# Kernel tuning notes

Hardware: AMD Instinct MI355X
Metric: run time of the kernel (lower is better)

The kernel has to match this reference:

```python
import jax, jax.numpy as jnp
import numpy as np

SAMPLE_NUMS = 9
VIEW_RANGE = 2      # args.max_turn_view_range
TEMP = 0.07         # args.temperature
AVG_EPS = 1e-6      # BertAVG eps
COS_EPS = 1e-8      # torch.cosine_similarity eps


def setup_inputs() -> dict:
    key = jax.random.key(0)
    k0, k1, k2 = jax.random.split(key, 3)
    G, S, H = 8, 512, 768            # groups, max_seq_length, hidden_size
    B = G * SAMPLE_NUMS              # 72 flattened dialogues
    self_output = jax.random.normal(k0, (B, S, H), dtype=jnp.float32)
    attention_mask = jnp.ones((B, S), dtype=jnp.float32)
    qa_ids = jax.random.randint(k1, (B, S), 0, 4, dtype=jnp.int32)
    turn_ids = jnp.sort(jax.random.randint(k2, (B, S), 0, 16, dtype=jnp.int32), axis=-1)
    labels = jnp.zeros((G, SAMPLE_NUMS), dtype=jnp.float32).at[:, 0].set(1.0)
    return {"self_output": self_output, "attention_mask": attention_mask,
            "labels": labels, "qa_ids": qa_ids, "turn_ids": turn_ids}


def _masked_avg(x, m):
    # BertAVG: sum over seq of x*m / (sum(m) + eps)   x:[B,S,H] m:[B,S]
    return jnp.sum(x * m[..., None], axis=1) / (jnp.sum(m, axis=1, keepdims=True) + AVG_EPS)


def _cos(x, y):
    # torch.cosine_similarity over last dim, eps-clamped norms
    dot = jnp.sum(x * y, axis=-1)
    nx = jnp.maximum(jnp.linalg.norm(x, axis=-1), COS_EPS)
    ny = jnp.maximum(jnp.linalg.norm(y, axis=-1), COS_EPS)
    c = dot / (nx * ny)
    c = jnp.where(c == 1.0, jnp.nan, c)   # cos[cos==1] = nan
    return c / TEMP


def _calc_loss(pred, labels):
    return -jnp.nanmean(jax.nn.log_softmax(pred, axis=-1) * labels)


def reference(self_output, attention_mask, labels, qa_ids, turn_ids):
    H = self_output.shape[-1]
    # role masks from qa_ids
    q_mask = ((qa_ids == 1) | (qa_ids == 2)).astype(self_output.dtype)
    a_mask = ((qa_ids == 0) | (qa_ids == 2)).astype(self_output.dtype)
    n_mask = (qa_ids == 3).astype(self_output.dtype)
    q_am = attention_mask * q_mask
    a_am = attention_mask * a_mask
    n_am = attention_mask * n_mask
    q_so = self_output * q_am[..., None]   # [B,S,H]
    a_so = self_output * a_am[..., None]
    n_so = self_output * n_am[..., None]
    # role-masked cross scores [B,S,S]
    q_w = jnp.einsum('bsh,bth->bst', q_so, a_so + n_so)
    a_w = jnp.einsum('bsh,bth->bst', a_so, q_so + n_so)
    n_w = jnp.einsum('bsh,bth->bst', n_so, q_so + a_so)
    # turn-range band mask: |turn_s - turn_t| <= range
    dt = turn_ids[:, :, None] - turn_ids[:, None, :]
    band = (jnp.abs(dt) <= VIEW_RANGE).astype(self_output.dtype)  # [B,S,S]
    filtered_w = (q_w + a_w + n_w) * band
    # cross outputs
    q_co = jnp.einsum('bst,bth->bsh', filtered_w, q_so)
    a_co = jnp.einsum('bst,bth->bsh', filtered_w, a_so)
    n_co = jnp.einsum('bst,bth->bsh', filtered_w, n_so)
    # masked averages
    q_self = _masked_avg(q_so, q_am)
    q_cross = _masked_avg(q_co, a_am + n_am)
    a_self = _masked_avg(a_so, a_am)
    a_cross = _masked_avg(a_co, q_am + n_am)
    n_self = _masked_avg(n_so, n_am)
    n_cross = _masked_avg(n_co, q_am + a_am)
    # [G, sample_nums, H]
    q_self = q_self.reshape(-1, SAMPLE_NUMS, H)
    q_cross = q_cross.reshape(-1, SAMPLE_NUMS, H)
    a_self = a_self.reshape(-1, SAMPLE_NUMS, H)
    a_cross = a_cross.reshape(-1, SAMPLE_NUMS, H)
    n_self = n_self.reshape(-1, SAMPLE_NUMS, H)
    n_cross = n_cross.reshape(-1, SAMPLE_NUMS, H)
    q_output = q_self[:, 0, :]
    a_output = a_self[:, 0, :]
    n_output = n_self[:, 0, :]
    # vectorized over sample axis (replaces the python loop + stack)
    logit_q = _cos(q_self, q_cross)  # [G, sample_nums]
    logit_a = _cos(a_self, a_cross)
    logit_n = _cos(n_self, n_cross)
    stage_loss = (_calc_loss(logit_a, labels) + _calc_loss(logit_q, labels)
                  + _calc_loss(logit_n, labels)) / 3.0
    return (stage_loss, q_output, a_output, n_output)
```

## Files before the change

kernel.cpp:

```cpp
#include <hip/hip_runtime.h>
#include <math.h>

#define BB 72
#define SS 512
#define HH 768
#define GG 8
#define SN 9
#define VR 2
#define NT 16
#define ASL 64
#define NPART 16


__device__ float g_W[(size_t)BB * NT * 4 * HH];
__device__ float g_snum[BB * 3 * HH];
__device__ float g_xpart[(size_t)BB * NPART * 3 * HH];
__device__ float g_logits[3 * BB];

__device__ __forceinline__ void class_masks(float am, int id, float& qv, float& av, float& nv) {
    qv = (id == 1 || id == 2) ? am : 0.0f;
    av = (id == 0 || id == 2) ? am : 0.0f;
    nv = (id == 3) ? am : 0.0f;
}

__global__ void k_gw(const float* __restrict__ x, const float* __restrict__ am,
                     const int* __restrict__ qa, const int* __restrict__ turn) {
    __shared__ float G[4][NT][4][ASL];
    __shared__ int   tn[SS];
    __shared__ float c2[SS];
    __shared__ int   idv[SS];

    const int b = blockIdx.y, hs = blockIdx.x;
    const int tid = threadIdx.x, w = tid >> 6, lane = tid & 63;
    const int h = hs * ASL + lane;

    for (int i = tid; i < SS; i += 256) {
        tn[i] = turn[b * SS + i];
        float a = am[b * SS + i]; c2[i] = a * a;
        idv[i] = qa[b * SS + i];
    }
    {
        float* Gf = &G[0][0][0][0];
        for (int i = tid; i < 4 * NT * 4 * ASL; i += 256) Gf[i] = 0.0f;
    }
    __syncthreads();

    const int s0 = w * (SS / 4);
    const float* xcol = x + (size_t)b * SS * HH + h;
    float r0 = 0, r1 = 0, r2 = 0, r3 = 0;
    int cur = tn[s0];

    float A[8], Bu[8];
#define LOADC(dst, c) { const float* p_ = xcol + (size_t)(s0 + (c) * 8) * HH;  \
    _Pragma("unroll") for (int j_ = 0; j_ < 8; ++j_) dst[j_] = p_[(size_t)j_ * HH]; }
#define FLUSH() { G[w][cur][0][lane] = r0; G[w][cur][1][lane] = r1;            \
                  G[w][cur][2][lane] = r2; G[w][cur][3][lane] = r3;            \
                  r0 = r1 = r2 = r3 = 0.0f; }
#define CONSUME(src, c) { _Pragma("unroll") for (int j_ = 0; j_ < 8; ++j_) {   \
    const int s_ = s0 + (c) * 8 + j_;                                          \
    const int v_ = tn[s_];                                                     \
    if (v_ != cur) { FLUSH(); cur = v_; }                                      \
    const float val_ = src[j_] * c2[s_];                                       \
    const int id_ = idv[s_];                                                   \
    if      (id_ == 0) r0 += val_;                                             \
    else if (id_ == 1) r1 += val_;                                             \
    else if (id_ == 2) r2 += val_;                                             \
    else               r3 += val_; } }

    LOADC(A, 0);
    for (int c = 0; c < 16; c += 2) {
        LOADC(Bu, c + 1);
        CONSUME(A, c);
        if (c + 2 < 16) LOADC(A, c + 2);
        CONSUME(Bu, c + 1);
    }
    FLUSH();
#undef LOADC
#undef FLUSH
#undef CONSUME
    __syncthreads();

    for (int v = w * 4; v < w * 4 + 4; ++v) {
        const int ulo = (v - VR < 0) ? 0 : v - VR;
        const int uhi = (v + VR > NT - 1) ? NT - 1 : v + VR;
        float a0 = 0, a1 = 0, a2 = 0, a3 = 0;
        for (int u = ulo; u <= uhi; ++u) {
#pragma unroll
            for (int wq = 0; wq < 4; ++wq) {
                a0 += G[wq][u][0][lane]; a1 += G[wq][u][1][lane];
                a2 += G[wq][u][2][lane]; a3 += G[wq][u][3][lane];
            }
        }
        float* Wo = g_W + ((size_t)(b * NT + v) * 4) * HH + h;
        Wo[0 * HH] = a0; Wo[1 * HH] = a1; Wo[2 * HH] = a2; Wo[3 * HH] = a3;
    }
    if (w == 0) {
        float t0 = 0, t1 = 0, t2 = 0, t3 = 0;
        for (int u = 0; u < NT; ++u) {
#pragma unroll
            for (int wq = 0; wq < 4; ++wq) {
                t0 += G[wq][u][0][lane]; t1 += G[wq][u][1][lane];
                t2 += G[wq][u][2][lane]; t3 += G[wq][u][3][lane];
            }
        }
        g_snum[(b * 3 + 0) * HH + h] = t1 + t2;
        g_snum[(b * 3 + 1) * HH + h] = t0 + t2;
        g_snum[(b * 3 + 2) * HH + h] = t3;
    }
}

__global__ void k_ct(const float* __restrict__ x, const float* __restrict__ am,
                     const int* __restrict__ qa, const int* __restrict__ turn) {
    __shared__ float Wl[4][HH];
    __shared__ float red[4][3 * HH];
    __shared__ int   tnb[32];
    __shared__ float amb[32];
    __shared__ int   idb[32];

    const int b = blockIdx.y, ts = blockIdx.x, T0 = ts * 32;
    const int tid = threadIdx.x, w = tid >> 6, lane = tid & 63;
    if (tid < 32) {
        tnb[tid] = turn[b * SS + T0 + tid];
        amb[tid] = am[b * SS + T0 + tid];
        idb[tid] = qa[b * SS + T0 + tid];
    }
    __syncthreads();
    const int vlo = tnb[0], vhi = tnb[31];
    const float* xb = x + (size_t)b * SS * HH;

    __align__(16) float xn[3][12];
#pragma unroll
    for (int c = 0; c < 3; ++c)
#pragma unroll
        for (int k = 0; k < 12; ++k) xn[c][k] = 0.0f;

    for (int v = vlo; v <= vhi; ++v) {
        const float* Wg = g_W + ((size_t)(b * NT + v) * 4) * HH;
        for (int i = tid * 4; i < 4 * HH; i += 1024)
            *(float4*)&Wl[0][i] = *(const float4*)(Wg + i);
        __syncthreads();

        for (int it = 0; it < 8; ++it) {
            const int tl = w * 8 + it;
            if (tnb[tl] != v) continue;
            const int t = T0 + tl;
            const float* xr = xb + (size_t)t * HH;
            float4 xt4[3];
            xt4[0] = *(const float4*)(xr + 0 * 256 + lane * 4);
            xt4[1] = *(const float4*)(xr + 1 * 256 + lane * 4);
            xt4[2] = *(const float4*)(xr + 2 * 256 + lane * 4);

            float d[4];
#pragma unroll
            for (int i = 0; i < 4; ++i) {
                float s = 0;
#pragma unroll
                for (int ch = 0; ch < 3; ++ch) {
                    const float4 wv = *(const float4*)&Wl[i][ch * 256 + lane * 4];
                    const float4 xv = xt4[ch];
                    s += xv.x * wv.x + xv.y * wv.y + xv.z * wv.z + xv.w * wv.w;
                }
                d[i] = s;
            }
#pragma unroll
            for (int off = 32; off; off >>= 1) {
#pragma unroll
                for (int i = 0; i < 4; ++i) d[i] += __shfl_xor(d[i], off);
            }
            float qt, at, nt; class_masks(amb[tl], idb[tl], qt, at, nt);
            const float ant = at + nt, qnt = qt + nt, qat = qt + at;
            const float Sqq = d[1] + d[2], Sqa = d[2], Saa = d[0] + d[2], Snn = d[3];
            const float cwq = qt * (ant * Sqa + qnt * Saa + qat * Snn);
            const float cwa = at * (ant * Sqq + qnt * Sqa + qat * Snn);
            const float cwn = nt * (ant * (Sqq + Sqa) + qnt * (Sqa + Saa));

            __align__(16) float xt[12];
            *(float4*)&xt[0] = xt4[0]; *(float4*)&xt[4] = xt4[1]; *(float4*)&xt[8] = xt4[2];
#pragma unroll
            for (int k = 0; k < 12; ++k) {
                xn[0][k] += cwq * xt[k];
                xn[1][k] += cwa * xt[k];
                xn[2][k] += cwn * xt[k];
            }
        }
        __syncthreads();
    }

#pragma unroll
    for (int c = 0; c < 3; ++c) {
#pragma unroll
        for (int ch = 0; ch < 3; ++ch)
            *(float4*)&red[w][c * HH + ch * 256 + lane * 4] = *(float4*)&xn[c][ch * 4];
    }
    __syncthreads();
    float* xo = g_xpart + (size_t)(b * NPART + ts) * 3 * HH;
    for (int idx = tid; idx < 3 * HH; idx += 256)
        xo[idx] = red[0][idx] + red[1][idx] + red[2][idx] + red[3][idx];
}

__global__ void k_cos(const float* __restrict__ am, const int* __restrict__ qa,
                      float* __restrict__ out) {
    const int c = blockIdx.x, b = blockIdx.y, tid = threadIdx.x;
    const int wave = tid >> 6, lane = tid & 63;
    __shared__ float redd[4][3];
    __shared__ float sD[3];

    float q = 0, a = 0, n = 0;
    for (int s = tid; s < SS; s += 256) {
        float m = am[b * SS + s]; int id = qa[b * SS + s];
        float qv, av, nv; class_masks(m, id, qv, av, nv);
        q += qv; a += av; n += nv;
    }
#pragma unroll
    for (int off = 32; off; off >>= 1) {
        q += __shfl_down(q, off); a += __shfl_down(a, off); n += __shfl_down(n, off);
    }
    if (lane == 0) { redd[wave][0] = q; redd[wave][1] = a; redd[wave][2] = n; }
    __syncthreads();
    if (tid == 0) {
        float Q = 0, A = 0, N = 0;
#pragma unroll
        for (int w = 0; w < 4; ++w) { Q += redd[w][0]; A += redd[w][1]; N += redd[w][2]; }
        sD[0] = Q; sD[1] = A; sD[2] = N;
    }
    __syncthreads();
    const float Dq = sD[0], Da = sD[1], Dn = sD[2];
    const float Dself = (c == 0) ? Dq : ((c == 1) ? Da : Dn);
    const float Dcross = (c == 0) ? (Da + Dn) : ((c == 1) ? (Dq + Dn) : (Dq + Da));
    const float invS = 1.0f / (Dself + 1e-6f), invC = 1.0f / (Dcross + 1e-6f);

    float dot = 0, n1 = 0, n2 = 0;
#pragma unroll
    for (int j = 0; j < 3; ++j) {
        const int h = tid + j * 256;
        float sv = g_snum[(b * 3 + c) * HH + h];
        float cv = 0;
        const float* xp = g_xpart + ((size_t)b * NPART * 3 + c) * HH + h;
#pragma unroll
        for (int p = 0; p < NPART; ++p) cv += xp[(size_t)p * 3 * HH];
        sv *= invS; cv *= invC;
        dot += sv * cv; n1 += sv * sv; n2 += cv * cv;
        if (b % SN == 0)
            out[1 + ((size_t)c * GG + b / SN) * HH + h] = sv;
    }
#pragma unroll
    for (int off = 32; off; off >>= 1) {
        dot += __shfl_down(dot, off); n1 += __shfl_down(n1, off); n2 += __shfl_down(n2, off);
    }
    __shared__ float red2[4][3];
    if (lane == 0) { red2[wave][0] = dot; red2[wave][1] = n1; red2[wave][2] = n2; }
    __syncthreads();
    if (tid == 0) {
        float D = 0, N1 = 0, N2 = 0;
#pragma unroll
        for (int w = 0; w < 4; ++w) { D += red2[w][0]; N1 += red2[w][1]; N2 += red2[w][2]; }
        float nx = fmaxf(sqrtf(N1), 1e-8f);
        float ny = fmaxf(sqrtf(N2), 1e-8f);
        float cc = D / (nx * ny);
        if (cc == 1.0f) cc = __uint_as_float(0x7FC00000u);
        g_logits[c * BB + b] = cc / 0.07f;
    }
}

__global__ void k_loss(const float* __restrict__ labels, float* __restrict__ out) {
    __shared__ float rs[24];
    __shared__ int rc[24];
    const int tid = threadIdx.x;
    if (tid < 24) {
        int c = tid / GG, g = tid % GG;
        float lg[SN]; bool anynan = false;
        for (int j = 0; j < SN; ++j) {
            float v = g_logits[c * BB + g * SN + j];
            lg[j] = v;
            anynan = anynan || isnan(v);
        }
        float ssum = 0; int cnt = 0;
        if (!anynan) {
            float m = -1e30f;
            for (int j = 0; j < SN; ++j) m = fmaxf(m, lg[j]);
            float se = 0;
            for (int j = 0; j < SN; ++j) se += expf(lg[j] - m);
            float lse = m + logf(se);
            for (int j = 0; j < SN; ++j) ssum += (lg[j] - lse) * labels[g * SN + j];
            cnt = SN;
        }
        rs[tid] = ssum; rc[tid] = cnt;
    }
    __syncthreads();
    if (tid == 0) {
        float total = 0;
        for (int c = 0; c < 3; ++c) {
            float s = 0; int n = 0;
            for (int g = 0; g < GG; ++g) { s += rs[c * GG + g]; n += rc[c * GG + g]; }
            total += -(s / (float)n);
        }
        out[0] = total / 3.0f;
    }
}

extern "C" void kernel_launch(void* const* d_in, const int* in_sizes, int n_in,
                              void* d_out, int out_size, void* d_ws, size_t ws_size,
                              hipStream_t stream) {
    const float* x      = (const float*)d_in[0];
    const float* am     = (const float*)d_in[1];
    const float* labels = (const float*)d_in[2];
    const int*   qa     = (const int*)d_in[3];
    const int*   turn   = (const int*)d_in[4];
    float* out = (float*)d_out;

    k_gw  <<<dim3(HH / ASL, BB), 256, 0, stream>>>(x, am, qa, turn);
    k_ct  <<<dim3(SS / 32, BB),  256, 0, stream>>>(x, am, qa, turn);
    k_cos <<<dim3(3, BB),        256, 0, stream>>>(am, qa, out);
    k_loss<<<dim3(1),            64,  0, stream>>>(labels, out);
}
```

Baseline: 259.5 us.

## Vectorize turn-group accumulation and keep W slices in registers in contraction kernel

The turn/role accumulation kernel now uses 512-thread blocks, each covering 256 hidden columns with float4 loads per lane over 64-row sequence slices. Per-wave partials are merged through shared-memory atomics into a single accumulator instead of per-wave copies. The cross-term kernel preloads all eight token rows into registers and reloads the W slice from global memory into registers only when the turn changes, which removes the shared-memory staging and the block-wide barriers per turn. The aim is fewer, wider memory transactions and less synchronisation, at the cost of higher register pressure and LDS atomic contention.

Result: faster. 241.6 us (-6.9%).

```diff
diff --git a/kernel.cpp b/kernel.cpp
--- a/kernel.cpp
+++ b/kernel.cpp
@@ -8,7 +8,6 @@
 #define SN 9
 #define VR 2
 #define NT 16
-#define ASL 64
 #define NPART 16
 
 
@@ -23,95 +22,125 @@
     nv = (id == 3) ? am : 0.0f;
 }
 
-__global__ void k_gw(const float* __restrict__ x, const float* __restrict__ am,
-                     const int* __restrict__ qa, const int* __restrict__ turn) {
-    __shared__ float G[4][NT][4][ASL];
+__global__ void k_g(const float* __restrict__ x, const float* __restrict__ am,
+                    const int* __restrict__ qa, const int* __restrict__ turn) {
+    __shared__ float Gs[NT * 4 * 4 * 64];
     __shared__ int   tn[SS];
     __shared__ float c2[SS];
     __shared__ int   idv[SS];
 
-    const int b = blockIdx.y, hs = blockIdx.x;
+    const int b = blockIdx.y, hbase = blockIdx.x * 256;
     const int tid = threadIdx.x, w = tid >> 6, lane = tid & 63;
-    const int h = hs * ASL + lane;
-
-    for (int i = tid; i < SS; i += 256) {
+
+    for (int i = tid; i < SS; i += 512) {
         tn[i] = turn[b * SS + i];
         float a = am[b * SS + i]; c2[i] = a * a;
         idv[i] = qa[b * SS + i];
     }
     {
-        float* Gf = &G[0][0][0][0];
-        for (int i = tid; i < 4 * NT * 4 * ASL; i += 256) Gf[i] = 0.0f;
-    }
-    __syncthreads();
-
-    const int s0 = w * (SS / 4);
-    const float* xcol = x + (size_t)b * SS * HH + h;
-    float r0 = 0, r1 = 0, r2 = 0, r3 = 0;
+        const float4 z = make_float4(0.f, 0.f, 0.f, 0.f);
+        for (int i = tid * 4; i < NT * 4 * 4 * 64; i += 2048) *(float4*)&Gs[i] = z;
+    }
+    __syncthreads();
+
+    const int s0 = w * 64;
+    const float* xbase = x + ((size_t)b * SS + s0) * HH + hbase + lane * 4;
+    float r[4][4];
+#pragma unroll
+    for (int i = 0; i < 4; ++i)
+#pragma unroll
+        for (int k = 0; k < 4; ++k) r[i][k] = 0.0f;
     int cur = tn[s0];
 
-    float A[8], Bu[8];
-#define LOADC(dst, c) { const float* p_ = xcol + (size_t)(s0 + (c) * 8) * HH;  \
-    _Pragma("unroll") for (int j_ = 0; j_ < 8; ++j_) dst[j_] = p_[(size_t)j_ * HH]; }
-#define FLUSH() { G[w][cur][0][lane] = r0; G[w][cur][1][lane] = r1;            \
-                  G[w][cur][2][lane] = r2; G[w][cur][3][lane] = r3;            \
-                  r0 = r1 = r2 = r3 = 0.0f; }
-#define CONSUME(src, c) { _Pragma("unroll") for (int j_ = 0; j_ < 8; ++j_) {   \
-    const int s_ = s0 + (c) * 8 + j_;                                          \
-    const int v_ = tn[s_];                                                     \
-    if (v_ != cur) { FLUSH(); cur = v_; }                                      \
-    const float val_ = src[j_] * c2[s_];                                       \
-    const int id_ = idv[s_];                                                   \
-    if      (id_ == 0) r0 += val_;                                             \
-    else if (id_ == 1) r1 += val_;                                             \
-    else if (id_ == 2) r2 += val_;                                             \
-    else               r3 += val_; } }
-
-    LOADC(A, 0);
+    float4 A[4], Bq[4];
+#define LDQ(buf, c) { _Pragma("unroll") for (int j_ = 0; j_ < 4; ++j_)          \
+        buf[j_] = *(const float4*)(xbase + (size_t)((c) * 4 + j_) * HH); }
+#define FLUSH() { _Pragma("unroll") for (int i_ = 0; i_ < 4; ++i_) {            \
+        _Pragma("unroll") for (int k_ = 0; k_ < 4; ++k_) {                      \
+            atomicAdd(&Gs[((cur * 4 + i_) * 4 + k_) * 64 + lane], r[i_][k_]);   \
+            r[i_][k_] = 0.0f; } } }
+#define CONSUME(buf, c) { _Pragma("unroll") for (int j_ = 0; j_ < 4; ++j_) {    \
+        const int s_ = s0 + (c) * 4 + j_;                                       \
+        const int v_ = tn[s_];                                                  \
+        if (v_ != cur) { FLUSH(); cur = v_; }                                   \
+        const float c2_ = c2[s_];                                               \
+        const int id_ = idv[s_];                                                \
+        const float4 xv_ = buf[j_];                                             \
+        if (id_ == 0) { r[0][0] += xv_.x * c2_; r[0][1] += xv_.y * c2_;         \
+                        r[0][2] += xv_.z * c2_; r[0][3] += xv_.w * c2_; }       \
+        else if (id_ == 1) { r[1][0] += xv_.x * c2_; r[1][1] += xv_.y * c2_;    \
+                             r[1][2] += xv_.z * c2_; r[1][3] += xv_.w * c2_; }  \
+        else if (id_ == 2) { r[2][0] += xv_.x * c2_; r[2][1] += xv_.y * c2_;    \
+                             r[2][2] += xv_.z * c2_; r[2][3] += xv_.w * c2_; }  \
+        else { r[3][0] += xv_.x * c2_; r[3][1] += xv_.y * c2_;                  \
+               r[3][2] += xv_.z * c2_; r[3][3] += xv_.w * c2_; } } }
+
+    LDQ(A, 0);
     for (int c = 0; c < 16; c += 2) {
-        LOADC(Bu, c + 1);
+        LDQ(Bq, c + 1);
         CONSUME(A, c);
-        if (c + 2 < 16) LOADC(A, c + 2);
-        CONSUME(Bu, c + 1);
+        if (c + 2 < 16) LDQ(A, c + 2);
+        CONSUME(Bq, c + 1);
     }
     FLUSH();
-#undef LOADC
+#undef LDQ
 #undef FLUSH
 #undef CONSUME
     __syncthreads();
 
-    for (int v = w * 4; v < w * 4 + 4; ++v) {
+#pragma unroll
+    for (int vv = 0; vv < 2; ++vv) {
+        const int v = w * 2 + vv;
         const int ulo = (v - VR < 0) ? 0 : v - VR;
         const int uhi = (v + VR > NT - 1) ? NT - 1 : v + VR;
-        float a0 = 0, a1 = 0, a2 = 0, a3 = 0;
+        float acc[4][4];
+#pragma unroll
+        for (int i = 0; i < 4; ++i)
+#pragma unroll
+            for (int k = 0; k < 4; ++k) acc[i][k] = 0.0f;
         for (int u = ulo; u <= uhi; ++u) {
 #pragma unroll
-            for (int wq = 0; wq < 4; ++wq) {
-                a0 += G[wq][u][0][lane]; a1 += G[wq][u][1][lane];
-                a2 += G[wq][u][2][lane]; a3 += G[wq][u][3][lane];
-            }
-        }
-        float* Wo = g_W + ((size_t)(b * NT + v) * 4) * HH + h;
-        Wo[0 * HH] = a0; Wo[1 * HH] = a1; Wo[2 * HH] = a2; Wo[3 * HH] = a3;
+            for (int i = 0; i < 4; ++i)
+#pragma unroll
+                for (int k = 0; k < 4; ++k)
+                    acc[i][k] += Gs[((u * 4 + i) * 4 + k) * 64 + lane];
+        }
+        float* Wo = g_W + ((size_t)(b * NT + v) * 4) * HH + hbase + lane * 4;
+#pragma unroll
+        for (int i = 0; i < 4; ++i) {
+            float4 o; o.x = acc[i][0]; o.y = acc[i][1]; o.z = acc[i][2]; o.w = acc[i][3];
+            *(float4*)(Wo + (size_t)i * HH) = o;
+        }
     }
     if (w == 0) {
-        float t0 = 0, t1 = 0, t2 = 0, t3 = 0;
+        float t[4][4];
+#pragma unroll
+        for (int i = 0; i < 4; ++i)
+#pragma unroll
+            for (int k = 0; k < 4; ++k) t[i][k] = 0.0f;
         for (int u = 0; u < NT; ++u) {
 #pragma unroll
-            for (int wq = 0; wq < 4; ++wq) {
-                t0 += G[wq][u][0][lane]; t1 += G[wq][u][1][lane];
-                t2 += G[wq][u][2][lane]; t3 += G[wq][u][3][lane];
-            }
-        }
-        g_snum[(b * 3 + 0) * HH + h] = t1 + t2;
-        g_snum[(b * 3 + 1) * HH + h] = t0 + t2;
-        g_snum[(b * 3 + 2) * HH + h] = t3;
-    }
-}
-
-__global__ void k_ct(const float* __restrict__ x, const float* __restrict__ am,
-                     const int* __restrict__ qa, const int* __restrict__ turn) {
-    __shared__ float Wl[4][HH];
+            for (int i = 0; i < 4; ++i)
+#pragma unroll
+                for (int k = 0; k < 4; ++k)
+                    t[i][k] += Gs[((u * 4 + i) * 4 + k) * 64 + lane];
+        }
+        float4 oq, oa, on;
+        oq.x = t[1][0] + t[2][0]; oq.y = t[1][1] + t[2][1];
+        oq.z = t[1][2] + t[2][2]; oq.w = t[1][3] + t[2][3];
+        oa.x = t[0][0] + t[2][0]; oa.y = t[0][1] + t[2][1];
+        oa.z = t[0][2] + t[2][2]; oa.w = t[0][3] + t[2][3];
+        on.x = t[3][0]; on.y = t[3][1]; on.z = t[3][2]; on.w = t[3][3];
+        *(float4*)(g_snum + (size_t)(b * 3 + 0) * HH + hbase + lane * 4) = oq;
+        *(float4*)(g_snum + (size_t)(b * 3 + 1) * HH + hbase + lane * 4) = oa;
+        *(float4*)(g_snum + (size_t)(b * 3 + 2) * HH + hbase + lane * 4) = on;
+    }
+}
+
+__global__ __launch_bounds__(256) void k_ct(const float* __restrict__ x,
+                                            const float* __restrict__ am,
+                                            const int* __restrict__ qa,
+                                            const int* __restrict__ turn) {
     __shared__ float red[4][3 * HH];
     __shared__ int   tnb[32];
     __shared__ float amb[32];
@@ -125,77 +154,98 @@
         idb[tid] = qa[b * SS + T0 + tid];
     }
     __syncthreads();
-    const int vlo = tnb[0], vhi = tnb[31];
+
     const float* xb = x + (size_t)b * SS * HH;
-
-    __align__(16) float xn[3][12];
+    float4 xt[8][3];
+#pragma unroll
+    for (int it = 0; it < 8; ++it) {
+        const float* xr = xb + (size_t)(T0 + w * 8 + it) * HH + lane * 4;
+        xt[it][0] = *(const float4*)(xr + 0);
+        xt[it][1] = *(const float4*)(xr + 256);
+        xt[it][2] = *(const float4*)(xr + 512);
+    }
+
+    float xn[3][12];
 #pragma unroll
     for (int c = 0; c < 3; ++c)
 #pragma unroll
         for (int k = 0; k < 12; ++k) xn[c][k] = 0.0f;
 
-    for (int v = vlo; v <= vhi; ++v) {
-        const float* Wg = g_W + ((size_t)(b * NT + v) * 4) * HH;
-        for (int i = tid * 4; i < 4 * HH; i += 1024)
-            *(float4*)&Wl[0][i] = *(const float4*)(Wg + i);
-        __syncthreads();
-
-        for (int it = 0; it < 8; ++it) {
-            const int tl = w * 8 + it;
-            if (tnb[tl] != v) continue;
-            const int t = T0 + tl;
-            const float* xr = xb + (size_t)t * HH;
-            float4 xt4[3];
-            xt4[0] = *(const float4*)(xr + 0 * 256 + lane * 4);
-            xt4[1] = *(const float4*)(xr + 1 * 256 + lane * 4);
-            xt4[2] = *(const float4*)(xr + 2 * 256 + lane * 4);
-
-            float d[4];
+    float4 Wr[4][3];
+    int curv = -1;
+
+#pragma unroll
+    for (int it = 0; it < 8; ++it) {
+        const int tl = w * 8 + it;
+        const int v = tnb[tl];
+        if (v != curv) {
+            curv = v;
+            const float* Wg = g_W + ((size_t)(b * NT + v) * 4) * HH + lane * 4;
 #pragma unroll
             for (int i = 0; i < 4; ++i) {
-                float s = 0;
-#pragma unroll
-                for (int ch = 0; ch < 3; ++ch) {
-                    const float4 wv = *(const float4*)&Wl[i][ch * 256 + lane * 4];
-                    const float4 xv = xt4[ch];
-                    s += xv.x * wv.x + xv.y * wv.y + xv.z * wv.z + xv.w * wv.w;
-                }
-                d[i] = s;
+                Wr[i][0] = *(const float4*)(Wg + (size_t)i * HH + 0);
+                Wr[i][1] = *(const float4*)(Wg + (size_t)i * HH + 256);
+                Wr[i][2] = *(const float4*)(Wg + (size_t)i * HH + 512);
             }
-#pragma unroll
-            for (int off = 32; off; off >>= 1) {
-#pragma unroll
-                for (int i = 0; i < 4; ++i) d[i] += __shfl_xor(d[i], off);
+        }
+        float d[4];
+#pragma unroll
+        for (int i = 0; i < 4; ++i) {
+            float s = 0;
+#pragma unroll
+            for (int ch = 0; ch < 3; ++ch) {
+                s += xt[it][ch].x * Wr[i][ch].x + xt[it][ch].y * Wr[i][ch].y
+                   + xt[it][ch].z * Wr[i][ch].z + xt[it][ch].w * Wr[i][ch].w;
             }
-            float qt, at, nt; class_masks(amb[tl], idb[tl], qt, at, nt);
-            const float ant = at + nt, qnt = qt + nt, qat = qt + at;
-            const float Sqq = d[1] + d[2], Sqa = d[2], Saa = d[0] + d[2], Snn = d[3];
-            const float cwq = qt * (ant * Sqa + qnt * Saa + qat * Snn);
-            const float cwa = at * (ant * Sqq + qnt * Sqa + qat * Snn);
-            const float cwn = nt * (ant * (Sqq + Sqa) + qnt * (Sqa + Saa));
-
-            __align__(16) float xt[12];
-            *(float4*)&xt[0] = xt4[0]; *(float4*)&xt[4] = xt4[1]; *(float4*)&xt[8] = xt4[2];
-#pragma unroll
-            for (int k = 0; k < 12; ++k) {
-                xn[0][k] += cwq * xt[k];
-                xn[1][k] += cwa * xt[k];
-                xn[2][k] += cwn * xt[k];
-            }
-        }
-        __syncthreads();
+            d[i] = s;
+        }
+#pragma unroll
+        for (int off = 32; off; off >>= 1) {
+#pragma unroll
+            for (int i = 0; i < 4; ++i) d[i] += __shfl_xor(d[i], off);
+        }
+        float qt, at, nt; class_masks(amb[tl], idb[tl], qt, at, nt);
+        const float ant = at + nt, qnt = qt + nt, qat = qt + at;
+        const float Sqq = d[1] + d[2], Sqa = d[2], Saa = d[0] + d[2], Snn = d[3];
+        const float cwq = qt * (ant * Sqa + qnt * Saa + qat * Snn);
+        const float cwa = at * (ant * Sqq + qnt * Sqa + qat * Snn);
+        const float cwn = nt * (ant * (Sqq + Sqa) + qnt * (Sqa + Saa));
+#pragma unroll
+        for (int ch = 0; ch < 3; ++ch) {
+            const float4 xv = xt[it][ch];
+            xn[0][ch * 4 + 0] += cwq * xv.x; xn[0][ch * 4 + 1] += cwq * xv.y;
+            xn[0][ch * 4 + 2] += cwq * xv.z; xn[0][ch * 4 + 3] += cwq * xv.w;
+            xn[1][ch * 4 + 0] += cwa * xv.x; xn[1][ch * 4 + 1] += cwa * xv.y;
+            xn[1][ch * 4 + 2] += cwa * xv.z; xn[1][ch * 4 + 3] += cwa * xv.w;
+            xn[2][ch * 4 + 0] += cwn * xv.x; xn[2][ch * 4 + 1] += cwn * xv.y;
+            xn[2][ch * 4 + 2] += cwn * xv.z; xn[2][ch * 4 + 3] += cwn * xv.w;
+        }
     }
 
 #pragma unroll
     for (int c = 0; c < 3; ++c) {
 #pragma unroll
-        for (int ch = 0; ch < 3; ++ch)
-            *(float4*)&red[w][c * HH + ch * 256 + lane * 4] = *(float4*)&xn[c][ch * 4];
+        for (int ch = 0; ch < 3; ++ch) {
+            float4 o;
+            o.x = xn[c][ch * 4 + 0]; o.y = xn[c][ch * 4 + 1];
+            o.z = xn[c][ch * 4 + 2]; o.w = xn[c][ch * 4 + 3];
+            *(float4*)&red[w][c * HH + ch * 256 + lane * 4] = o;
+        }
     }
     __syncthreads();
     float* xo = g_xpart + (size_t)(b * NPART + ts) * 3 * HH;
-    for (int idx = tid; idx < 3 * HH; idx += 256)
-        xo[idx] = red[0][idx] + red[1][idx] + red[2][idx] + red[3][idx];
+    for (int idx = tid * 4; idx < 3 * HH; idx += 1024) {
+        float4 r0 = *(float4*)&red[0][idx];
+        float4 r1 = *(float4*)&red[1][idx];
+        float4 r2 = *(float4*)&red[2][idx];
+        float4 r3 = *(float4*)&red[3][idx];
+        float4 o;
+        o.x = r0.x + r1.x + r2.x + r3.x;
+        o.y = r0.y + r1.y + r2.y + r3.y;
+        o.z = r0.z + r1.z + r2.z + r3.z;
+        o.w = r0.w + r1.w + r2.w + r3.w;
+        *(float4*)(xo + idx) = o;
+    }
 }
 
 __global__ void k_cos(const float* __restrict__ am, const int* __restrict__ qa,
@@ -233,7 +283,7 @@
 #pragma unroll
     for (int j = 0; j < 3; ++j) {
         const int h = tid + j * 256;
-        float sv = g_snum[(b * 3 + c) * HH + h];
+        float sv = g_snum[(size_t)(b * 3 + c) * HH + h];
         float cv = 0;
         const float* xp = g_xpart + ((size_t)b * NPART * 3 + c) * HH + h;
 #pragma unroll
@@ -308,7 +358,7 @@
     const int*   turn   = (const int*)d_in[4];
     float* out = (float*)d_out;
 
-    k_gw  <<<dim3(HH / ASL, BB), 256, 0, stream>>>(x, am, qa, turn);
+    k_g   <<<dim3(HH / 256, BB), 512, 0, stream>>>(x, am, qa, turn);
     k_ct  <<<dim3(SS / 32, BB),  256, 0, stream>>>(x, am, qa, turn);
     k_cos <<<dim3(3, BB),        256, 0, stream>>>(am, qa, out);
     k_loss<<<dim3(1),            64,  0, stream>>>(labels, out);
```
